# Performance work log

Measured on AMD Instinct MI355X. Metric: run time of the kernel, lower is better.

The kernel has to match this reference:

```python
import jax, jax.numpy as jnp
import numpy as np

EMBED_DIM = 2048
NUM_HEADS = 16
HEAD_DIM = EMBED_DIM // NUM_HEADS  # 128
GROUP = 256
NEG = -1e9


def setup_inputs() -> dict:
    key = jax.random.key(0)
    ks = jax.random.split(key, 4)
    B, N, C = 2, 8192, EMBED_DIM
    s = 1.0 / np.sqrt(C).astype(np.float32)
    return {
        "x": jax.random.normal(ks[0], (B, N, C), jnp.float32),
        "Wq": jax.random.normal(ks[1], (C, C), jnp.float32) * s,
        "bq": jnp.zeros((C,), jnp.float32),
        "Wk": jax.random.normal(ks[2], (C, C), jnp.float32) * s,
        "bk": jnp.zeros((C,), jnp.float32),
        "Wv": jax.random.normal(ks[3], (C, C), jnp.float32) * s,
        "bv": jnp.zeros((C,), jnp.float32),
    }


def _s2_attn(x, Wq, bq, Wk, bk, Wv, bv):
    B, N, C = x.shape
    H, hd, gs = NUM_HEADS, HEAD_DIM, GROUP
    G = N // gs
    half = H // 2

    def heads(t):  # [B,N,C] -> [B,H,N,hd]
        return t.reshape(B, N, H, hd).transpose(0, 2, 1, 3)

    q = heads(x @ Wq.T + bq)
    k = heads(x @ Wk.T + bk)
    v = heads(x @ Wv.T + bv)

    def shift(t, s):  # shift second half of heads along sequence
        return jnp.concatenate([t[:, :half], jnp.roll(t[:, half:], s, axis=2)], axis=1)

    q, k, v = shift(q, -(gs // 2)), shift(k, -(gs // 2)), shift(v, -(gs // 2))

    # group-local attention: [B,H,G,gs,hd]
    qg = q.reshape(B, H, G, gs, hd)
    kg = k.reshape(B, H, G, gs, hd)
    vg = v.reshape(B, H, G, gs, hd)

    scores = jnp.einsum("bhgqd,bhgkd->bhgqk", qg, kg) / np.sqrt(hd).astype(x.dtype)
    causal = jnp.triu(jnp.ones((gs, gs), bool), 1)  # mask strictly-upper triangle
    scores = jnp.where(causal, NEG, scores)
    attn = jax.nn.softmax(scores, axis=-1)
    out = jnp.einsum("bhgqk,bhgkd->bhgqd", attn, vg).reshape(B, H, N, hd)

    out = shift(out, gs // 2)  # un-shift the shifted heads
    return out.transpose(0, 2, 1, 3).reshape(B, N, C)


def reference(x, Wq, bq, Wk, bk, Wv, bv):
    return _s2_attn(x, Wq, bq, Wk, bk, Wv, bv)
```

## Files before the change

### kernel.cpp

```cpp
#include <hip/hip_runtime.h>
#include <hip/hip_bf16.h>

#define NSEQ 8192
#define CDIM 2048
#define NHEAD 16
#define HD 128

typedef short short8 __attribute__((ext_vector_type(8)));
typedef short short4v __attribute__((ext_vector_type(4)));
typedef float float4v __attribute__((ext_vector_type(4)));

__device__ __forceinline__ short f2bf(float f) {
    __hip_bfloat16 h = __float2bfloat16(f);
    return *reinterpret_cast<short*>(&h);
}

__device__ __forceinline__ void async_load16(const short* g, short* l) {
    __builtin_amdgcn_global_load_lds((const __attribute__((address_space(1))) void*)g,
                                     (__attribute__((address_space(3))) void*)l,
                                     16, 0, 0);
}

#define X8 (33554432 / 8)
#define W8 (4194304 / 8)

__global__ __launch_bounds__(256) void cvt_all(
    const float* __restrict__ x, const float* __restrict__ wq,
    const float* __restrict__ wk, const float* __restrict__ wv,
    short* __restrict__ xb, short* __restrict__ wqb,
    short* __restrict__ wkb, short* __restrict__ wvb)
{
    const size_t i = (size_t)blockIdx.x * blockDim.x + threadIdx.x;
    const float* src;
    short* dst;
    size_t off;
    if (i < X8)              { src = x;  dst = xb;  off = i; }
    else if (i < X8 + W8)    { src = wq; dst = wqb; off = i - X8; }
    else if (i < X8 + 2*W8)  { src = wk; dst = wkb; off = i - X8 - W8; }
    else                     { src = wv; dst = wvb; off = i - X8 - 2*(size_t)W8; }
    const float4v a = ((const float4v*)src)[off * 2];
    const float4v b = ((const float4v*)src)[off * 2 + 1];
    short8 o;
    for (int j = 0; j < 4; j++) { o[j] = f2bf(a[j]); o[4 + j] = f2bf(b[j]); }
    ((short8*)dst)[off] = o;
}

__global__ __launch_bounds__(256, 2) void qkv_gemm(
    const short* __restrict__ x,
    const short* __restrict__ Wq, const float* __restrict__ bq,
    const short* __restrict__ Wk, const float* __restrict__ bk,
    const short* __restrict__ Wv, const float* __restrict__ bv,
    float* __restrict__ qout, short* __restrict__ kt, short* __restrict__ vt)
{
    __shared__ short As[128 * 32];
    __shared__ short Bs[128 * 32];

    const int tid  = threadIdx.x;
    const int wave = tid >> 6;
    const int lane = tid & 63;
    const int quad = lane >> 4;
    const int l15  = lane & 15;
    const int wm   = wave >> 1;
    const int wn   = wave & 1;

    const int m0  = blockIdx.x * 128;
    const int mat = blockIdx.y >> 4;
    const int h   = blockIdx.y & 15;
    const int n0  = h * HD;

    const short* W    = (mat == 0) ? Wq : (mat == 1) ? Wk : Wv;
    const float* bias = (mat == 0) ? bq : (mat == 1) ? bk : bv;

    const int srow = lane >> 2;
    const int scol = (lane & 3) * 8;

    const float4v fzero = {0.f, 0.f, 0.f, 0.f};
    float4v acc[4][4];
    for (int i = 0; i < 4; i++)
        for (int j = 0; j < 4; j++)
            acc[i][j] = fzero;

    for (int k0 = 0; k0 < CDIM; k0 += 32) {
        __syncthreads();
        for (int c = 0; c < 2; c++) {
            const int chunk = wave * 2 + c;
            const int row   = chunk * 16 + srow;
            async_load16(x + (size_t)(m0 + row) * CDIM + k0 + scol, &As[chunk * 512]);
            async_load16(W + (size_t)(n0 + row) * CDIM + k0 + scol, &Bs[chunk * 512]);
        }
        __syncthreads();

        short8 af[4], bf[4];
        for (int i = 0; i < 4; i++)
            af[i] = *(const short8*)&As[(wm * 64 + i * 16 + l15) * 32 + quad * 8];
        for (int j = 0; j < 4; j++)
            bf[j] = *(const short8*)&Bs[(wn * 64 + j * 16 + l15) * 32 + quad * 8];
        for (int i = 0; i < 4; i++)
            for (int j = 0; j < 4; j++)
                acc[i][j] = __builtin_amdgcn_mfma_f32_16x16x32_bf16(af[i], bf[j],
                                                                    acc[i][j], 0, 0, 0);
    }

    float bvals[4];
    for (int j = 0; j < 4; j++)
        bvals[j] = bias[n0 + wn * 64 + j * 16 + l15];

    for (int i = 0; i < 4; i++) {
        for (int j = 0; j < 4; j++) {
            const int d = wn * 64 + j * 16 + l15;
            for (int r = 0; r < 4; r++) {
                const int m   = m0 + wm * 64 + i * 16 + quad * 4 + r;
                const int b   = m >> 13;
                const int seq = m & (NSEQ - 1);
                const float v = acc[i][j][r] + bvals[j];
                if (mat == 0) {
                    qout[((size_t)(b * NSEQ + seq) << 11) + n0 + d] = v;
                } else {
                    short* outp = (mat == 1) ? kt : vt;
                    outp[(((size_t)(b * NHEAD + h) * NSEQ + seq) << 7) + d] = f2bf(v);
                }
            }
        }
    }
}

__global__ __launch_bounds__(512, 2) void s2_attn(const float* qsrc,
                                                  const short* __restrict__ kt,
                                                  const short* __restrict__ vt,
                                                  float* out)
{
    __shared__ short Ks[64 * 136];
    __shared__ short Vs[64 * 132];
    __shared__ short Ps[8][32 * 40];

    const int bx = blockIdx.x;
    const int g  = bx & 31;
    const int h  = (bx >> 5) & 15;
    const int b  = bx >> 9;
    const int shift = (h >= 8) ? 128 : 0;
    const int sbase = g * 256 + shift;

    const int tid  = threadIdx.x;
    const int wave = tid >> 6;
    const int lane = tid & 63;
    const int quad = lane >> 4;
    const int l15  = lane & 15;

    const size_t bh = ((size_t)b * NHEAD + h) * NSEQ;
    const short* kg = kt + bh * HD;
    const short* vg = vt + bh * HD;

    const int mt0 = wave * 2;

    short8 qf[2][4];
    for (int im = 0; im < 2; im++) {
        const int row = (mt0 + im) * 16 + l15;
        const int p   = (sbase + row) & (NSEQ - 1);
        const float* qr = qsrc + (((size_t)(b * NSEQ + p)) << 11) + h * HD;
        for (int ks = 0; ks < 4; ks++) {
            const float4v qa = *(const float4v*)(qr + ks * 32 + quad * 8);
            const float4v qb = *(const float4v*)(qr + ks * 32 + quad * 8 + 4);
            short8 f;
            for (int j = 0; j < 4; j++) { f[j] = f2bf(qa[j]); f[4 + j] = f2bf(qb[j]); }
            qf[im][ks] = f;
        }
    }

    const float4v fzero = {0.f, 0.f, 0.f, 0.f};
    float4v o[2][8];
    for (int im = 0; im < 2; im++)
        for (int dt = 0; dt < 8; dt++)
            o[im][dt] = fzero;
    float rs[2][4] = {{0.f, 0.f, 0.f, 0.f}, {0.f, 0.f, 0.f, 0.f}};

    for (int kc = 0; kc < 4; kc++) {
        __syncthreads();
        for (int c = 0; c < 2; c++) {
            const int id   = tid + c * 512;
            const int row  = id >> 4;
            const int colb = (id & 15) * 8;
            const int p    = (sbase + kc * 64 + row) & (NSEQ - 1);
            *(short8*)&Ks[row * 136 + colb] = *(const short8*)(kg + (size_t)p * HD + colb);
        }
        for (int c = 0; c < 4; c++) {
            const int id   = tid + c * 512;
            const int row  = id >> 5;
            const int colb = (id & 31) * 4;
            const int p    = (sbase + kc * 64 + row) & (NSEQ - 1);
            *(short4v*)&Vs[row * 132 + colb] = *(const short4v*)(vg + (size_t)p * HD + colb);
        }
        __syncthreads();

        float4v s[2][4];
        for (int im = 0; im < 2; im++)
            for (int nn = 0; nn < 4; nn++)
                s[im][nn] = fzero;
        for (int nn = 0; nn < 4; nn++) {
            short8 kf[4];
            for (int ks = 0; ks < 4; ks++)
                kf[ks] = *(const short8*)&Ks[(nn * 16 + l15) * 136 + ks * 32 + quad * 8];
            for (int im = 0; im < 2; im++)
                for (int ks = 0; ks < 4; ks++)
                    s[im][nn] = __builtin_amdgcn_mfma_f32_16x16x32_bf16(
                        qf[im][ks], kf[ks], s[im][nn], 0, 0, 0);
        }

        for (int half = 0; half < 2; half++) {
            for (int im = 0; im < 2; im++) {
                const int qpos = (mt0 + im) * 16 + quad * 4;
                for (int nn2 = 0; nn2 < 2; nn2++) {
                    const int nn   = half * 2 + nn2;
                    const int kpos = kc * 64 + nn * 16 + l15;
                    for (int r = 0; r < 4; r++) {
                        const float sv = s[im][nn][r] * 0.088388347648318447f;
                        const float pv = (kpos > qpos + r)
                                             ? 0.f
                                             : __expf(fminf(sv, 30.f));
                        rs[im][r] += pv;
                        Ps[wave][(im * 16 + quad * 4 + r) * 40 + nn2 * 16 + l15] = f2bf(pv);
                    }
                }
            }
            __syncthreads();
            short8 pf[2];
            for (int im = 0; im < 2; im++)
                pf[im] = *(const short8*)&Ps[wave][(im * 16 + l15) * 40 + quad * 8];
            for (int dt = 0; dt < 8; dt++) {
                short8 vf;
                for (int jj = 0; jj < 8; jj++)
                    vf[jj] = Vs[(half * 32 + quad * 8 + jj) * 132 + dt * 16 + l15];
                for (int im = 0; im < 2; im++)
                    o[im][dt] = __builtin_amdgcn_mfma_f32_16x16x32_bf16(
                        pf[im], vf, o[im][dt], 0, 0, 0);
            }
            __syncthreads();
        }
    }

    for (int im = 0; im < 2; im++)
        for (int r = 0; r < 4; r++) {
            float v = rs[im][r];
            v += __shfl_xor(v, 1);
            v += __shfl_xor(v, 2);
            v += __shfl_xor(v, 4);
            v += __shfl_xor(v, 8);
            rs[im][r] = v;
        }

    for (int im = 0; im < 2; im++) {
        for (int r = 0; r < 4; r++) {
            const int row = (mt0 + im) * 16 + quad * 4 + r;
            const int p   = (sbase + row) & (NSEQ - 1);
            const float inv = 1.f / rs[im][r];
            const size_t obase = (((size_t)(b * NSEQ + p)) << 11) + h * HD;
            for (int dt = 0; dt < 8; dt++)
                out[obase + dt * 16 + l15] = o[im][dt][r] * inv;
        }
    }
}

extern "C" void kernel_launch(void* const* d_in, const int* in_sizes, int n_in,
                              void* d_out, int out_size, void* d_ws, size_t ws_size,
                              hipStream_t stream) {
    (void)in_sizes; (void)n_in; (void)out_size; (void)ws_size;
    const float* x  = (const float*)d_in[0];
    const float* Wq = (const float*)d_in[1];
    const float* bq = (const float*)d_in[2];
    const float* Wk = (const float*)d_in[3];
    const float* bk = (const float*)d_in[4];
    const float* Wv = (const float*)d_in[5];
    const float* bv = (const float*)d_in[6];

    short* xb  = (short*)d_ws;
    short* wqb = xb  + (size_t)33554432;
    short* wkb = wqb + (size_t)4194304;
    short* wvb = wkb + (size_t)4194304;
    short* kt  = wvb + (size_t)4194304;
    short* vt  = kt  + (size_t)33554432;

    float* outp = (float*)d_out;

    cvt_all<<<dim3(22528), 256, 0, stream>>>(x, Wq, Wk, Wv, xb, wqb, wkb, wvb);
    qkv_gemm<<<dim3(128, 48), 256, 0, stream>>>(xb, wqb, bq, wkb, bk, wvb, bv,
                                                outp, kt, vt);
    s2_attn<<<dim3(1024), 512, 0, stream>>>(outp, kt, vt, outp);
}
```

Before: 876.3 us.

## Rewrite QKV GEMM as 256x256-tile double-buffered pipelined MFMA kernel

Replaces the 128x128 tile, single-buffered, fully synchronized QKV GEMM with a 512-thread kernel computing 256x256 tiles. It uses K=64 steps, double-buffered LDS filled by async global-to-LDS loads, and XOR-swizzled LDS addressing to avoid bank conflicts. Loads are interleaved with MFMA phases using explicit barriers, waitcnts and s_setprio, and block ids are remapped for L2 locality. The aim is to hide memory latency and raise arithmetic intensity of the dominant GEMM. In exchange it needs far more registers and LDS (128 KB), and the hand-written wait counts are fragile.

After: 774.2 us. 11.7% less time.

```diff
diff --git a/kernel.cpp b/kernel.cpp
--- a/kernel.cpp
+++ b/kernel.cpp
@@ -45,79 +45,217 @@
     ((short8*)dst)[off] = o;
 }
 
-__global__ __launch_bounds__(256, 2) void qkv_gemm(
-    const short* __restrict__ x,
+#define PBAR()  asm volatile("s_barrier" ::: "memory")
+#define LGKM0() do { asm volatile("s_waitcnt lgkmcnt(0)" ::: "memory"); \
+                     __builtin_amdgcn_sched_barrier(0); } while (0)
+#define VMC4()  asm volatile("s_waitcnt vmcnt(4)" ::: "memory")
+
+#define MFMA(d, x, y) d = __builtin_amdgcn_mfma_f32_16x16x32_bf16(x, y, d, 0, 0, 0)
+
+__global__ __launch_bounds__(512, 2) void qkv_gemm8(
+    const short* __restrict__ xb,
     const short* __restrict__ Wq, const float* __restrict__ bq,
     const short* __restrict__ Wk, const float* __restrict__ bk,
     const short* __restrict__ Wv, const float* __restrict__ bv,
     float* __restrict__ qout, short* __restrict__ kt, short* __restrict__ vt)
 {
-    __shared__ short As[128 * 32];
-    __shared__ short Bs[128 * 32];
+    __shared__ short lds[2][2][256 * 64];
 
     const int tid  = threadIdx.x;
-    const int wave = tid >> 6;
+    const int w    = tid >> 6;
     const int lane = tid & 63;
     const int quad = lane >> 4;
     const int l15  = lane & 15;
-    const int wm   = wave >> 1;
-    const int wn   = wave & 1;
-
-    const int m0  = blockIdx.x * 128;
-    const int mat = blockIdx.y >> 4;
-    const int h   = blockIdx.y & 15;
-    const int n0  = h * HD;
+    const int wm   = w >> 2;
+    const int wn   = w & 3;
+
+    const int id    = (blockIdx.x & 7) * 192 + (blockIdx.x >> 3);
+    const int mtile = id / 24;
+    const int rest  = id - mtile * 24;
+    const int mat   = rest >> 3;
+    const int ntile = rest & 7;
+    const int M0 = mtile << 8;
+    const int N0 = ntile << 8;
 
     const short* W    = (mat == 0) ? Wq : (mat == 1) ? Wk : Wv;
     const float* bias = (mat == 0) ? bq : (mat == 1) ? bk : bv;
-
-    const int srow = lane >> 2;
-    const int scol = (lane & 3) * 8;
-
-    const float4v fzero = {0.f, 0.f, 0.f, 0.f};
-    float4v acc[4][4];
-    for (int i = 0; i < 4; i++)
-        for (int j = 0; j < 4; j++)
-            acc[i][j] = fzero;
-
-    for (int k0 = 0; k0 < CDIM; k0 += 32) {
-        __syncthreads();
-        for (int c = 0; c < 2; c++) {
-            const int chunk = wave * 2 + c;
-            const int row   = chunk * 16 + srow;
-            async_load16(x + (size_t)(m0 + row) * CDIM + k0 + scol, &As[chunk * 512]);
-            async_load16(W + (size_t)(n0 + row) * CDIM + k0 + scol, &Bs[chunk * 512]);
-        }
-        __syncthreads();
-
-        short8 af[4], bf[4];
-        for (int i = 0; i < 4; i++)
-            af[i] = *(const short8*)&As[(wm * 64 + i * 16 + l15) * 32 + quad * 8];
-        for (int j = 0; j < 4; j++)
-            bf[j] = *(const short8*)&Bs[(wn * 64 + j * 16 + l15) * 32 + quad * 8];
-        for (int i = 0; i < 4; i++)
-            for (int j = 0; j < 4; j++)
-                acc[i][j] = __builtin_amdgcn_mfma_f32_16x16x32_bf16(af[i], bf[j],
-                                                                    acc[i][j], 0, 0, 0);
+    const short* Ab = xb + (size_t)M0 * CDIM;
+    const short* Bb = W  + (size_t)N0 * CDIM;
+
+    const int stg_row = tid >> 3;
+    const int stg_col = ((tid & 7) * 8) ^ (((tid >> 3) & 1) << 5) ^ (((tid >> 6) & 1) << 4);
+    const int cswz    = ((lane & 1) << 5) | (((lane >> 3) & 1) << 4);
+
+    float bvals[4];
+#pragma unroll
+    for (int j = 0; j < 4; ++j)
+        bvals[j] = bias[N0 + wn * 64 + j * 16 + l15];
+    asm volatile("s_waitcnt vmcnt(0)" ::: "memory");
+
+    float4v acc[8][4];
+#pragma unroll
+    for (int i = 0; i < 8; ++i)
+#pragma unroll
+        for (int j = 0; j < 4; ++j)
+            acc[i][j] = (float4v){0.f, 0.f, 0.f, 0.f};
+
+    auto stage = [&](int bufi, int ab, int h, int t, const short* src) {
+        short* l0 = &lds[bufi][ab][h * 8192 + w * 512];
+        const short* g = src + (size_t)(h * 128 + stg_row) * CDIM + t * 64 + stg_col;
+        async_load16(g, l0);
+        async_load16(g + (size_t)64 * CDIM, l0 + 4096);
+    };
+    auto ldA = [&](int bufi, int i, int ks) -> short8 {
+        const int row = wm * 128 + i * 16 + l15;
+        return *(const short8*)&lds[bufi][0][row * 64 + ((ks * 32 + quad * 8) ^ cswz)];
+    };
+    auto ldB = [&](int bufi, int j, int ks) -> short8 {
+        const int row = wn * 64 + j * 16 + l15;
+        return *(const short8*)&lds[bufi][1][row * 64 + ((ks * 32 + quad * 8) ^ cswz)];
+    };
+
+    stage(0, 0, 0, 0, Ab); stage(0, 0, 1, 0, Ab);
+    stage(0, 1, 0, 0, Bb); stage(0, 1, 1, 0, Bb);
+    stage(1, 1, 0, 1, Bb); stage(1, 1, 1, 1, Bb);
+    VMC4();
+    PBAR();
+
+    short8 a[4][2], b[4][2];
+    for (int it = 0; it < 16; ++it) {
+        const int t1 = 2 * it + 1;
+        const int t2 = (2 * it + 2 > 31) ? 31 : 2 * it + 2;
+        const int t3 = (2 * it + 3 > 31) ? 31 : 2 * it + 3;
+
+#pragma unroll
+        for (int i = 0; i < 4; ++i) { a[i][0] = ldA(0, i, 0); a[i][1] = ldA(0, i, 1); }
+#pragma unroll
+        for (int j = 0; j < 2; ++j) { b[j][0] = ldB(0, j, 0); b[j][1] = ldB(0, j, 1); }
+        stage(1, 0, 0, t1, Ab); stage(1, 0, 1, t1, Ab);
+        PBAR(); LGKM0();
+        __builtin_amdgcn_s_setprio(1);
+#pragma unroll
+        for (int i = 0; i < 4; ++i)
+#pragma unroll
+            for (int j = 0; j < 2; ++j) { MFMA(acc[i][j], a[i][0], b[j][0]);
+                                          MFMA(acc[i][j], a[i][1], b[j][1]); }
+        __builtin_amdgcn_s_setprio(0);
+        PBAR();
+
+#pragma unroll
+        for (int j = 2; j < 4; ++j) { b[j][0] = ldB(0, j, 0); b[j][1] = ldB(0, j, 1); }
+        PBAR(); LGKM0();
+        __builtin_amdgcn_s_setprio(1);
+#pragma unroll
+        for (int i = 0; i < 4; ++i)
+#pragma unroll
+            for (int j = 2; j < 4; ++j) { MFMA(acc[i][j], a[i][0], b[j][0]);
+                                          MFMA(acc[i][j], a[i][1], b[j][1]); }
+        __builtin_amdgcn_s_setprio(0);
+        PBAR();
+
+#pragma unroll
+        for (int i = 0; i < 4; ++i) { a[i][0] = ldA(0, 4 + i, 0); a[i][1] = ldA(0, 4 + i, 1); }
+        stage(0, 1, 0, t2, Bb);
+        PBAR(); LGKM0();
+        __builtin_amdgcn_s_setprio(1);
+#pragma unroll
+        for (int i = 0; i < 4; ++i)
+#pragma unroll
+            for (int j = 2; j < 4; ++j) { MFMA(acc[4 + i][j], a[i][0], b[j][0]);
+                                          MFMA(acc[4 + i][j], a[i][1], b[j][1]); }
+        __builtin_amdgcn_s_setprio(0);
+        PBAR();
+
+        stage(0, 1, 1, t2, Bb);
+        PBAR(); LGKM0();
+        __builtin_amdgcn_s_setprio(1);
+#pragma unroll
+        for (int i = 0; i < 4; ++i)
+#pragma unroll
+            for (int j = 0; j < 2; ++j) { MFMA(acc[4 + i][j], a[i][0], b[j][0]);
+                                          MFMA(acc[4 + i][j], a[i][1], b[j][1]); }
+        __builtin_amdgcn_s_setprio(0);
+        VMC4();
+        PBAR();
+
+#pragma unroll
+        for (int i = 0; i < 4; ++i) { a[i][0] = ldA(1, i, 0); a[i][1] = ldA(1, i, 1); }
+#pragma unroll
+        for (int j = 0; j < 2; ++j) { b[j][0] = ldB(1, j, 0); b[j][1] = ldB(1, j, 1); }
+        stage(0, 0, 0, t2, Ab); stage(0, 0, 1, t2, Ab);
+        PBAR(); LGKM0();
+        __builtin_amdgcn_s_setprio(1);
+#pragma unroll
+        for (int i = 0; i < 4; ++i)
+#pragma unroll
+            for (int j = 0; j < 2; ++j) { MFMA(acc[i][j], a[i][0], b[j][0]);
+                                          MFMA(acc[i][j], a[i][1], b[j][1]); }
+        __builtin_amdgcn_s_setprio(0);
+        PBAR();
+
+#pragma unroll
+        for (int j = 2; j < 4; ++j) { b[j][0] = ldB(1, j, 0); b[j][1] = ldB(1, j, 1); }
+        PBAR(); LGKM0();
+        __builtin_amdgcn_s_setprio(1);
+#pragma unroll
+        for (int i = 0; i < 4; ++i)
+#pragma unroll
+            for (int j = 2; j < 4; ++j) { MFMA(acc[i][j], a[i][0], b[j][0]);
+                                          MFMA(acc[i][j], a[i][1], b[j][1]); }
+        __builtin_amdgcn_s_setprio(0);
+        PBAR();
+
+#pragma unroll
+        for (int i = 0; i < 4; ++i) { a[i][0] = ldA(1, 4 + i, 0); a[i][1] = ldA(1, 4 + i, 1); }
+        stage(1, 1, 0, t3, Bb);
+        PBAR(); LGKM0();
+        __builtin_amdgcn_s_setprio(1);
+#pragma unroll
+        for (int i = 0; i < 4; ++i)
+#pragma unroll
+            for (int j = 2; j < 4; ++j) { MFMA(acc[4 + i][j], a[i][0], b[j][0]);
+                                          MFMA(acc[4 + i][j], a[i][1], b[j][1]); }
+        __builtin_amdgcn_s_setprio(0);
+        PBAR();
+
+        stage(1, 1, 1, t3, Bb);
+        PBAR(); LGKM0();
+        __builtin_amdgcn_s_setprio(1);
+#pragma unroll
+        for (int i = 0; i < 4; ++i)
+#pragma unroll
+            for (int j = 0; j < 2; ++j) { MFMA(acc[4 + i][j], a[i][0], b[j][0]);
+                                          MFMA(acc[4 + i][j], a[i][1], b[j][1]); }
+        __builtin_amdgcn_s_setprio(0);
+        VMC4();
+        PBAR();
     }
 
-    float bvals[4];
-    for (int j = 0; j < 4; j++)
-        bvals[j] = bias[n0 + wn * 64 + j * 16 + l15];
-
-    for (int i = 0; i < 4; i++) {
-        for (int j = 0; j < 4; j++) {
-            const int d = wn * 64 + j * 16 + l15;
-            for (int r = 0; r < 4; r++) {
-                const int m   = m0 + wm * 64 + i * 16 + quad * 4 + r;
-                const int b   = m >> 13;
-                const int seq = m & (NSEQ - 1);
-                const float v = acc[i][j][r] + bvals[j];
-                if (mat == 0) {
-                    qout[((size_t)(b * NSEQ + seq) << 11) + n0 + d] = v;
-                } else {
-                    short* outp = (mat == 1) ? kt : vt;
-                    outp[(((size_t)(b * NHEAD + h) * NSEQ + seq) << 7) + d] = f2bf(v);
+#pragma unroll
+    for (int j = 0; j < 4; ++j) {
+        const int n = N0 + wn * 64 + j * 16 + l15;
+        if (mat == 0) {
+#pragma unroll
+            for (int i = 0; i < 8; ++i) {
+                const int mrow = M0 + wm * 128 + i * 16 + quad * 4;
+#pragma unroll
+                for (int r = 0; r < 4; ++r)
+                    qout[((size_t)(mrow + r) << 11) + n] = acc[i][j][r] + bvals[j];
+            }
+        } else {
+            short* outp = (mat == 1) ? kt : vt;
+            const int h = n >> 7;
+            const int d = n & (HD - 1);
+#pragma unroll
+            for (int i = 0; i < 8; ++i) {
+                const int mrow = M0 + wm * 128 + i * 16 + quad * 4;
+#pragma unroll
+                for (int r = 0; r < 4; ++r) {
+                    const int m  = mrow + r;
+                    const int bb = m >> 13;
+                    const int sq = m & (NSEQ - 1);
+                    outp[(((size_t)(bb * NHEAD + h) * NSEQ + sq) << 7) + d] =
+                        f2bf(acc[i][j][r] + bvals[j]);
                 }
             }
         }
@@ -281,7 +419,7 @@
     float* outp = (float*)d_out;
 
     cvt_all<<<dim3(22528), 256, 0, stream>>>(x, Wq, Wk, Wv, xb, wqb, wkb, wvb);
-    qkv_gemm<<<dim3(128, 48), 256, 0, stream>>>(xb, wqb, bq, wkb, bk, wvb, bv,
-                                                outp, kt, vt);
+    qkv_gemm8<<<dim3(1536), 512, 0, stream>>>(xb, wqb, bq, wkb, bk, wvb, bv,
+                                              outp, kt, vt);
     s2_attn<<<dim3(1024), 512, 0, stream>>>(outp, kt, vt, outp);
 }
```
